# Kernel tuning notes

Hardware: AMD Instinct MI355X
Metric: run time of the kernel (lower is better)

## Reference

```python
import jax, jax.numpy as jnp
import numpy as np

# model constants (from source: PRE/COMM/OUT sizes; chosen: G, D, E, T, NF)
G, D, E, T = 128, 64, 8, 4096          # group feats, per-elevator feats, n elevators, timesteps
PRE, CI, CH, OUT, NF = 256, 128, 128, 128, 64
ROUNDS, DROPOFF = 3, 0.333
IN = G + D                              # elevator_input_size = 192
OIN = 2 * CH + IN                       # out-LSTM input = 448


def _cell(x, h, c, Wih, Whh, b):
    # torch nn.LSTM cell, gate order i,f,g,o; b = b_ih + b_hh
    g = x @ Wih.T + h @ Whh.T + b
    i, f, gg, o = jnp.split(g, 4, axis=-1)
    c2 = jax.nn.sigmoid(f) * c + jax.nn.sigmoid(i) * jnp.tanh(gg)
    h2 = jax.nn.sigmoid(o) * jnp.tanh(c2)
    return h2, c2


def _forward(features, pre_h0, pre_c0, out_h0, out_c0,
             Wih_p0, Whh_p0, b_p0, Wih_p1, Whh_p1, b_p1, Wfc, bfc,
             Wih_c0, Whh_c0, b_c0, Wih_c1, Whh_c1, b_c1,
             Wih_o, Whh_o, b_o, Wtar, btar, Wdir, bdir):
    def step(carry, feat):
        pre_h, pre_c, out_h, out_c = carry
        group = feat[:G]
        ele = feat[G:].reshape(E, D)
        x = jnp.concatenate([jnp.broadcast_to(group, (E, G)), ele], axis=-1)  # [E, IN]
        # preprocess: 2-layer LSTM single step, batched over elevators
        h0, c0 = _cell(x, pre_h[:, 0], pre_c[:, 0], Wih_p0, Whh_p0, b_p0)
        h1, c1 = _cell(h0, pre_h[:, 1], pre_c[:, 1], Wih_p1, Whh_p1, b_p1)
        pre_out = jax.nn.leaky_relu(h1 @ Wfc.T + bfc, 0.05)                   # [E, CI]
        new_pre_h = jnp.stack([h0, h1], axis=1)
        new_pre_c = jnp.stack([c0, c1], axis=1)
        # alpha-decayed communication rounds: sequential scan over elevators
        ch = jnp.zeros((2, CH), jnp.float32)
        cc = jnp.zeros((2, CH), jnp.float32)
        alpha = 1.0
        for _ in range(ROUNDS):
            def comm_step(cs, xin, alpha=alpha):
                ch_, cc_ = cs
                h0n, c0n = _cell(xin, ch_[0], cc_[0], Wih_c0, Whh_c0, b_c0)
                h0b = (1.0 - alpha) * ch_[0] + alpha * h0n
                c0b = (1.0 - alpha) * cc_[0] + alpha * c0n
                h1n, c1n = _cell(h0b, ch_[1], cc_[1], Wih_c1, Whh_c1, b_c1)
                h1b = (1.0 - alpha) * ch_[1] + alpha * h1n
                c1b = (1.0 - alpha) * cc_[1] + alpha * c1n
                return (jnp.stack([h0b, h1b]), jnp.stack([c0b, c1b])), None
            (ch, cc), _ = jax.lax.scan(comm_step, (ch, cc), pre_out)
            alpha *= DROPOFF
        group_dec = cc.reshape(-1)                                            # [2*CH] = comm_c.flatten()
        out_in = jnp.concatenate([jnp.broadcast_to(group_dec, (E, 2 * CH)), x], axis=-1)  # [E, OIN]
        oh, oc = _cell(out_in, out_h, out_c, Wih_o, Whh_o, b_o)
        tar = jax.nn.softmax(oh @ Wtar.T + btar, axis=-1)                     # [E, NF]
        dr = jax.nn.softmax(oh @ Wdir.T + bdir, axis=-1)                      # [E, 3]
        return (new_pre_h, new_pre_c, oh, oc), (tar, dr)

    _, (tar_seq, dir_seq) = jax.lax.scan(step, (pre_h0, pre_c0, out_h0, out_c0), features)
    return tar_seq, dir_seq


def setup_inputs() -> dict:
    key = jax.random.key(0)
    ks = iter(jax.random.split(key, 32))
    p = lambda *s: jax.random.normal(next(ks), s, jnp.float32) * 0.05
    return {
        "features": jax.random.normal(next(ks), (T, G + E * D), jnp.float32),
        "pre_h0": jnp.zeros((E, 2, PRE), jnp.float32),
        "pre_c0": jnp.zeros((E, 2, PRE), jnp.float32),
        "out_h0": jnp.zeros((E, OUT), jnp.float32),
        "out_c0": jnp.zeros((E, OUT), jnp.float32),
        "Wih_p0": p(4 * PRE, IN), "Whh_p0": p(4 * PRE, PRE), "b_p0": p(4 * PRE),
        "Wih_p1": p(4 * PRE, PRE), "Whh_p1": p(4 * PRE, PRE), "b_p1": p(4 * PRE),
        "Wfc": p(CI, PRE), "bfc": p(CI),
        "Wih_c0": p(4 * CH, CI), "Whh_c0": p(4 * CH, CH), "b_c0": p(4 * CH),
        "Wih_c1": p(4 * CH, CH), "Whh_c1": p(4 * CH, CH), "b_c1": p(4 * CH),
        "Wih_o": p(4 * OUT, OIN), "Whh_o": p(4 * OUT, OUT), "b_o": p(4 * OUT),
        "Wtar": p(NF, OUT), "btar": p(NF),
        "Wdir": p(3, OUT), "bdir": p(3),
    }


def reference(features, pre_h0, pre_c0, out_h0, out_c0,
              Wih_p0, Whh_p0, b_p0, Wih_p1, Whh_p1, b_p1, Wfc, bfc,
              Wih_c0, Whh_c0, b_c0, Wih_c1, Whh_c1, b_c1,
              Wih_o, Whh_o, b_o, Wtar, btar, Wdir, bdir):
    return _forward(features, pre_h0, pre_c0, out_h0, out_c0,
                    Wih_p0, Whh_p0, b_p0, Wih_p1, Whh_p1, b_p1, Wfc, bfc,
                    Wih_c0, Whh_c0, b_c0, Wih_c1, Whh_c1, b_c1,
                    Wih_o, Whh_o, b_o, Wtar, btar, Wdir, bdir)
```

## Files before the change

### kernel.cpp

```cpp
#include <hip/hip_runtime.h>
#include <hip/hip_bf16.h>

#define T_   4096
#define E_   8
#define NCON 56

typedef unsigned long long ull;

__device__ __forceinline__ float sigm(float x)  { return 1.0f / (1.0f + __expf(-x)); }
__device__ __forceinline__ float tanh_(float x) { return 1.0f - 2.0f / (__expf(2.0f * x) + 1.0f); }

__device__ __forceinline__ ull aload64(const ull* p) {
  return __hip_atomic_load(p, __ATOMIC_RELAXED, __HIP_MEMORY_SCOPE_AGENT);
}
__device__ __forceinline__ int aload32(const int* p) {
  return __hip_atomic_load(p, __ATOMIC_RELAXED, __HIP_MEMORY_SCOPE_AGENT);
}
__device__ __forceinline__ float aloadf(const float* p) {
  return __hip_atomic_load(p, __ATOMIC_RELAXED, __HIP_MEMORY_SCOPE_AGENT);
}
__device__ __forceinline__ void lbar() {
  asm volatile("s_waitcnt lgkmcnt(0)\n\ts_barrier" ::: "memory");
}

#define FMA_8(ACC, W, VA, VB)                                   \
  ACC[0] = fmaf((W), (VA).x, ACC[0]); ACC[1] = fmaf((W), (VA).y, ACC[1]); \
  ACC[2] = fmaf((W), (VA).z, ACC[2]); ACC[3] = fmaf((W), (VA).w, ACC[3]); \
  ACC[4] = fmaf((W), (VB).x, ACC[4]); ACC[5] = fmaf((W), (VB).y, ACC[5]); \
  ACC[6] = fmaf((W), (VB).z, ACC[6]); ACC[7] = fmaf((W), (VB).w, ACC[7]);

__global__ void initK(const float* __restrict__ Wih_p0, const float* __restrict__ Whh_p0,
                      const float* __restrict__ Wih_p1, const float* __restrict__ Whh_p1,
                      const float* __restrict__ Wih_c0, const float* __restrict__ Whh_c0,
                      const float* __restrict__ Wih_c1, const float* __restrict__ Whh_c1,
                      const float* __restrict__ Wih_o,
                      float* wt_p0, float* wt_p1, float* wt_c0, float* wt_c1,
                      float* wt_o1, float* wt_o2, int* zbase) {
  const int NW = 458752 + 524288 + 131072 + 131072 + 131072 + 98304;
  const int NZ = 65536 + 16384 + 65536 + 65536 + 65536 + 16384;
  const int NTOT = NW + NZ;
  const int gsz = gridDim.x * blockDim.x;
  for (int i = blockIdx.x * blockDim.x + threadIdx.x; i < NTOT; i += gsz) {
    int idx = i;
    if (idx < 458752) { int k = idx >> 10, c = idx & 1023;
      int wg = c >> 5, r5 = c & 31, gate = r5 >> 3, jl = r5 & 7;
      int col = gate * 256 + wg * 8 + jl;
      wt_p0[idx] = (k < 192) ? Wih_p0[col * 192 + k] : Whh_p0[col * 256 + (k - 192)]; continue; }
    idx -= 458752;
    if (idx < 524288) { int k = idx >> 10, c = idx & 1023;
      int wg = c >> 5, r5 = c & 31, gate = r5 >> 3, jl = r5 & 7;
      int col = gate * 256 + wg * 8 + jl;
      wt_p1[idx] = (k < 256) ? Wih_p1[col * 256 + k] : Whh_p1[col * 256 + (k - 256)]; continue; }
    idx -= 524288;
    if (idx < 131072) { int k = idx >> 9, r = idx & 511;
      wt_c0[idx] = (k < 128) ? Wih_c0[r * 128 + k] : Whh_c0[r * 128 + (k - 128)]; continue; }
    idx -= 131072;
    if (idx < 131072) { int k = idx >> 9, r = idx & 511;
      wt_c1[idx] = (k < 128) ? Wih_c1[r * 128 + k] : Whh_c1[r * 128 + (k - 128)]; continue; }
    idx -= 131072;
    if (idx < 131072) { int k = idx >> 9, r = idx & 511;
      wt_o1[idx] = Wih_o[r * 448 + k]; continue; }
    idx -= 131072;
    if (idx < 98304) { int k = idx >> 9, r = idx & 511;
      wt_o2[idx] = Wih_o[r * 448 + 256 + k]; continue; }
    idx -= 98304;
    zbase[idx] = 0;
  }
}

__global__ void opre2K(const float* __restrict__ feat, const float* __restrict__ wt_o2,
                       __hip_bfloat16* __restrict__ opre2) {
  __shared__ float xb[192 * 8];
  const int t = blockIdx.x, tid = threadIdx.x;
  const float* ft = feat + (size_t)t * 640;
  for (int idx = tid; idx < 192 * 8; idx += 256) {
    int k = idx >> 3, e = idx & 7;
    xb[idx] = (k < 128) ? ft[k] : ft[128 + e * 64 + (k - 128)];
  }
  __syncthreads();
  const int r = tid;
  float A0[8] = {0,0,0,0,0,0,0,0};
  float A1[8] = {0,0,0,0,0,0,0,0};
  const float4* x4 = (const float4*)xb;
  #pragma unroll 2
  for (int k = 0; k < 192; ++k) {
    float w0 = wt_o2[k * 512 + r];
    float w1 = wt_o2[k * 512 + 256 + r];
    float4 a = x4[k * 2], b = x4[k * 2 + 1];
    FMA_8(A0, w0, a, b);
    FMA_8(A1, w1, a, b);
  }
  #pragma unroll
  for (int e = 0; e < 8; ++e) {
    opre2[((size_t)t * 8 + e) * 512 + r]       = __float2bfloat16(A0[e]);
    opre2[((size_t)t * 8 + e) * 512 + 256 + r] = __float2bfloat16(A1[e]);
  }
}

__device__ __forceinline__ void comm_cell(
    const float* __restrict__ wt, const float* __restrict__ bias,
    const float* xin, float* hL, float* cL, float* glb, float* hout,
    float alpha, int tid) {
  const int r = tid;
  float A0[8] = {0,0,0,0,0,0,0,0};
  float A1[8] = {0,0,0,0,0,0,0,0};
  const float4* x4 = (const float4*)xin;
  #pragma unroll 2
  for (int k = 0; k < 128; ++k) {
    float w0 = wt[k * 512 + r];
    float w1 = wt[k * 512 + 256 + r];
    float4 a = x4[k * 2], b = x4[k * 2 + 1];
    FMA_8(A0, w0, a, b);
    FMA_8(A1, w1, a, b);
  }
  const float4* h4 = (const float4*)hL;
  #pragma unroll 2
  for (int k = 0; k < 128; ++k) {
    float w0 = wt[(128 + k) * 512 + r];
    float w1 = wt[(128 + k) * 512 + 256 + r];
    float4 a = h4[k * 2], b = h4[k * 2 + 1];
    FMA_8(A0, w0, a, b);
    FMA_8(A1, w1, a, b);
  }
  {
    float4* g4 = (float4*)glb;
    g4[r * 2]             = make_float4(A0[0], A0[1], A0[2], A0[3]);
    g4[r * 2 + 1]         = make_float4(A0[4], A0[5], A0[6], A0[7]);
    g4[(256 + r) * 2]     = make_float4(A1[0], A1[1], A1[2], A1[3]);
    g4[(256 + r) * 2 + 1] = make_float4(A1[4], A1[5], A1[6], A1[7]);
  }
  __syncthreads();
  for (int idx = tid; idx < 1024; idx += 256) {
    int jj = idx >> 3, tt = idx & 7;
    float gi = glb[jj * 8 + tt]         + bias[jj];
    float gf = glb[(128 + jj) * 8 + tt] + bias[128 + jj];
    float gg = glb[(256 + jj) * 8 + tt] + bias[256 + jj];
    float go = glb[(384 + jj) * 8 + tt] + bias[384 + jj];
    float cold = cL[idx], hold = hL[idx];
    float c2 = sigm(gf) * cold + sigm(gi) * tanh_(gg);
    float h2 = sigm(go) * tanh_(c2);
    float hb = fmaf(alpha, h2 - hold, hold);
    float cb = fmaf(alpha, c2 - cold, cold);
    hL[idx] = hb; cL[idx] = cb;
    if (hout) hout[idx] = hb;
  }
  __syncthreads();
}

__launch_bounds__(256, 1)
__global__ void megaK(const float* __restrict__ feat,
                      const float* __restrict__ pre_h0, const float* __restrict__ pre_c0,
                      const float* __restrict__ wt_p0, const float* __restrict__ wt_p1,
                      const float* __restrict__ b_p0, const float* __restrict__ b_p1,
                      float* __restrict__ h0ring, float* __restrict__ h1ring,
                      float* __restrict__ h1all,
                      int* __restrict__ flagsA, int* __restrict__ flagB1,
                      int* __restrict__ flagsBC,
                      const float* __restrict__ Wfc, const float* __restrict__ bfc,
                      const float* __restrict__ wt_c0, const float* __restrict__ wt_c1,
                      const float* __restrict__ b_c0, const float* __restrict__ b_c1,
                      const float* __restrict__ wt_o1, const float* __restrict__ b_o,
                      float* __restrict__ opre1, int* __restrict__ flagC,
                      const __hip_bfloat16* __restrict__ opre2,
                      const float* __restrict__ Whh_o, const float* __restrict__ out_h0,
                      const float* __restrict__ out_c0, float* __restrict__ oh_g) {
  __shared__ float lds[38912];
  const int wg = blockIdx.x, tid = threadIdx.x;

  if (wg < 32) {
    float* wl   = lds;
    float* xbuf = lds + 14336;
    float* hsf  = lds + 15872;
    float* gl   = lds + 17920;
    const int r5 = tid & 31, kq = tid >> 5;
    for (int idx = tid; idx < 14336; idx += 256)
      wl[idx] = wt_p0[(size_t)(idx >> 5) * 1024 + wg * 32 + (idx & 31)];
    float creg = 0.f, bi = 0.f, bff = 0.f, bg = 0.f, bo = 0.f;
    if (tid < 64) {
      const int jl = tid >> 3, e = tid & 7, j = wg * 8 + jl;
      creg = pre_c0[(e * 2 + 0) * 256 + j];
      bi = b_p0[j]; bff = b_p0[256 + j]; bg = b_p0[512 + j]; bo = b_p0[768 + j];
    }
    for (int idx = tid; idx < 2048; idx += 256) {
      int k = idx >> 3, e = idx & 7;
      hsf[idx] = pre_h0[(e * 2 + 0) * 256 + k];
    }
    for (int idx = tid; idx < 1536; idx += 256) {
      int k = idx >> 3, e = idx & 7;
      xbuf[idx] = (k < 128) ? feat[k] : feat[128 + e * 64 + (k - 128)];
    }
    __syncthreads();
    float Ax[8] = {0,0,0,0,0,0,0,0};
    {
      const float4* x4 = (const float4*)xbuf;
      #pragma unroll
      for (int k = kq * 24; k < kq * 24 + 24; ++k) {
        float w = wl[k * 32 + r5];
        float4 a = x4[k * 2], b = x4[k * 2 + 1];
        FMA_8(Ax, w, a, b);
      }
    }
    for (int t = 0; t < T_; ++t) {
      float px[6];
      if (t + 1 < T_) {
        const float* ft1 = feat + (size_t)(t + 1) * 640;
        #pragma unroll
        for (int i = 0; i < 6; ++i) {
          int idx = tid + i * 256; int k = idx >> 3, e = idx & 7;
          px[i] = (k < 128) ? ft1[k] : ft1[128 + e * 64 + (k - 128)];
        }
      }
      float A[8];
      #pragma unroll
      for (int i = 0; i < 8; ++i) A[i] = Ax[i];
      {
        const float4* h4 = (const float4*)hsf;
        #pragma unroll
        for (int k2 = 0; k2 < 32; ++k2) {
          const int k = kq * 32 + k2;
          float w = wl[(192 + k) * 32 + r5];
          float4 a = h4[k * 2], b = h4[k * 2 + 1];
          FMA_8(A, w, a, b);
        }
      }
      {
        float4* g4 = (float4*)gl;
        g4[(kq * 32 + r5) * 2]     = make_float4(A[0], A[1], A[2], A[3]);
        g4[(kq * 32 + r5) * 2 + 1] = make_float4(A[4], A[5], A[6], A[7]);
      }
      if (t >= 24 && tid >= 224) {
        const int t2 = (t - 24) | 7;
        const int* fp = flagsBC + ((size_t)(t2 & 63) * 32 + (tid - 224)) * 32;
        while (aload32(fp) < t2 + 1) __builtin_amdgcn_s_sleep(16);
      }
      lbar();
      if (tid < 64) {
        float s0 = 0.f, s1 = 0.f, s2 = 0.f, s3 = 0.f;
        #pragma unroll
        for (int q = 0; q < 8; ++q) {
          s0 += gl[q * 256 + tid];       s1 += gl[q * 256 + 64 + tid];
          s2 += gl[q * 256 + 128 + tid]; s3 += gl[q * 256 + 192 + tid];
        }
        float c2 = sigm(s1 + bff) * creg + sigm(s0 + bi) * tanh_(s2 + bg);
        float h2 = sigm(s3 + bo) * tanh_(c2);
        creg = c2;
        __hip_atomic_store(&h0ring[(size_t)(t & 31) * 2048 + wg * 64 + tid], h2,
                           __ATOMIC_RELAXED, __HIP_MEMORY_SCOPE_AGENT);
        asm volatile("s_waitcnt vmcnt(0)" ::: "memory");
        if (tid == 0)
          __hip_atomic_store(&flagsA[((size_t)(t & 63) * 32 + wg) * 32], t + 1,
                             __ATOMIC_RELAXED, __HIP_MEMORY_SCOPE_AGENT);
      }
      if (t + 1 >= T_) break;
      #pragma unroll
      for (int i = 0; i < 6; ++i) xbuf[tid + i * 256] = px[i];
      if (tid >= 64 && tid < 96) {
        const int* fp = flagsA + ((size_t)(t & 63) * 32 + (tid - 64)) * 32;
        while (aload32(fp) < t + 1) __builtin_amdgcn_s_sleep(1);
      }
      lbar();
      ull v[4];
      {
        const ull* s8 = (const ull*)(h0ring + (size_t)(t & 31) * 2048);
        #pragma unroll
        for (int i = 0; i < 4; ++i) v[i] = aload64(s8 + tid * 4 + i);
      }
      #pragma unroll
      for (int i = 0; i < 8; ++i) Ax[i] = 0.f;
      {
        const float4* x4 = (const float4*)xbuf;
        #pragma unroll
        for (int k = kq * 24; k < kq * 24 + 24; ++k) {
          float w = wl[k * 32 + r5];
          float4 a = x4[k * 2], b = x4[k * 2 + 1];
          FMA_8(Ax, w, a, b);
        }
      }
      {
        ull* d8 = (ull*)hsf;
        #pragma unroll
        for (int i = 0; i < 4; ++i) d8[tid * 4 + i] = v[i];
      }
      lbar();
    }
  } else if (wg < 64) {
    const int wgl = wg - 32;
    float* wl  = lds;
    float* xh0 = lds + 16384;
    float* hsf = lds + 18432;
    float* gl  = lds + 20480;
    const int r5 = tid & 31, kq = tid >> 5;
    for (int idx = tid; idx < 16384; idx += 256)
      wl[idx] = wt_p1[(size_t)(idx >> 5) * 1024 + wgl * 32 + (idx & 31)];
    float creg = 0.f, bi = 0.f, bff = 0.f, bg = 0.f, bo = 0.f;
    if (tid < 64) {
      const int jl = tid >> 3, e = tid & 7, j = wgl * 8 + jl;
      creg = pre_c0[(e * 2 + 1) * 256 + j];
      bi = b_p1[j]; bff = b_p1[256 + j]; bg = b_p1[512 + j]; bo = b_p1[768 + j];
    }
    for (int idx = tid; idx < 2048; idx += 256) {
      int k = idx >> 3, e = idx & 7;
      hsf[idx] = pre_h0[(e * 2 + 1) * 256 + k];
    }
    __syncthreads();
    if (tid >= 64 && tid < 128) {
      const int lane = tid - 64;
      const int slot = lane >> 5, b = lane & 31;
      const int* fp = flagsA + ((size_t)slot * 32 + b) * 32;
      while (aload32(fp) < slot + 1) __builtin_amdgcn_s_sleep(1);
    }
    __syncthreads();
    ull v0[4];
    {
      const ull* s8 = (const ull*)h0ring;
      #pragma unroll
      for (int i = 0; i < 4; ++i) v0[i] = aload64(s8 + tid * 4 + i);
    }
    {
      ull* d8 = (ull*)xh0;
      #pragma unroll
      for (int i = 0; i < 4; ++i) d8[tid * 4 + i] = v0[i];
    }
    lbar();
    float Ax[8] = {0,0,0,0,0,0,0,0};
    {
      const float4* x4 = (const float4*)xh0;
      #pragma unroll
      for (int k = kq * 32; k < kq * 32 + 32; ++k) {
        float w = wl[k * 32 + r5];
        float4 a = x4[k * 2], b = x4[k * 2 + 1];
        FMA_8(Ax, w, a, b);
      }
    }
    {
      const ull* s8 = (const ull*)(h0ring + 2048);
      #pragma unroll
      for (int i = 0; i < 4; ++i) v0[i] = aload64(s8 + tid * 4 + i);
    }
    for (int t = 0; t < T_; ++t) {
      float A[8];
      #pragma unroll
      for (int i = 0; i < 8; ++i) A[i] = Ax[i];
      {
        const float4* h4 = (const float4*)hsf;
        #pragma unroll
        for (int k2 = 0; k2 < 32; ++k2) {
          const int k = kq * 32 + k2;
          float w = wl[(256 + k) * 32 + r5];
          float4 a = h4[k * 2], b = h4[k * 2 + 1];
          FMA_8(A, w, a, b);
        }
      }
      {
        float4* g4 = (float4*)gl;
        g4[(kq * 32 + r5) * 2]     = make_float4(A[0], A[1], A[2], A[3]);
        g4[(kq * 32 + r5) * 2 + 1] = make_float4(A[4], A[5], A[6], A[7]);
      }
      lbar();
      if (tid < 64) {
        float s0 = 0.f, s1 = 0.f, s2 = 0.f, s3 = 0.f;
        #pragma unroll
        for (int q = 0; q < 8; ++q) {
          s0 += gl[q * 256 + tid];       s1 += gl[q * 256 + 64 + tid];
          s2 += gl[q * 256 + 128 + tid]; s3 += gl[q * 256 + 192 + tid];
        }
        float c2 = sigm(s1 + bff) * creg + sigm(s0 + bi) * tanh_(s2 + bg);
        float h2 = sigm(s3 + bo) * tanh_(c2);
        creg = c2;
        __hip_atomic_store(&h1ring[(size_t)(t & 7) * 2048 + wgl * 64 + tid], h2,
                           __ATOMIC_RELAXED, __HIP_MEMORY_SCOPE_AGENT);
        asm volatile("s_waitcnt vmcnt(0)" ::: "memory");
        if (tid == 0)
          __hip_atomic_store(&flagB1[((size_t)(t & 63) * 32 + wgl) * 32], t + 1,
                             __ATOMIC_RELAXED, __HIP_MEMORY_SCOPE_AGENT);
        __hip_atomic_store(&h1all[(size_t)t * 2048 + wgl * 64 + tid], h2,
                           __ATOMIC_RELAXED, __HIP_MEMORY_SCOPE_AGENT);
        if ((t & 7) == 7) {
          asm volatile("s_waitcnt vmcnt(0)" ::: "memory");
          if (tid == 0)
            __hip_atomic_store(&flagsBC[((size_t)(t & 63) * 32 + wgl) * 32], t + 1,
                               __ATOMIC_RELAXED, __HIP_MEMORY_SCOPE_AGENT);
        }
      }
      if (t + 1 >= T_) break;
      if (tid >= 64 && tid < 128) {
        const int lane = tid - 64;
        if (lane < 32) {
          const int* fp = flagB1 + ((size_t)(t & 63) * 32 + lane) * 32;
          while (aload32(fp) < t + 1) __builtin_amdgcn_s_sleep(1);
        } else if (t + 2 < T_) {
          const int* fp = flagsA + ((size_t)((t + 2) & 63) * 32 + (lane - 32)) * 32;
          while (aload32(fp) < t + 3) __builtin_amdgcn_s_sleep(1);
        }
      }
      lbar();
      ull v1[4];
      {
        const ull* s8 = (const ull*)(h1ring + (size_t)(t & 7) * 2048);
        #pragma unroll
        for (int i = 0; i < 4; ++i) v1[i] = aload64(s8 + tid * 4 + i);
      }
      {
        ull* d8 = (ull*)xh0;
        #pragma unroll
        for (int i = 0; i < 4; ++i) d8[tid * 4 + i] = v0[i];
      }
      lbar();
      if (t + 2 < T_) {
        const ull* s8 = (const ull*)(h0ring + (size_t)((t + 2) & 31) * 2048);
        #pragma unroll
        for (int i = 0; i < 4; ++i) v0[i] = aload64(s8 + tid * 4 + i);
      }
      #pragma unroll
      for (int i = 0; i < 8; ++i) Ax[i] = 0.f;
      {
        const float4* x4 = (const float4*)xh0;
        #pragma unroll
        for (int k = kq * 32; k < kq * 32 + 32; ++k) {
          float w = wl[k * 32 + r5];
          float4 a = x4[k * 2], b = x4[k * 2 + 1];
          FMA_8(Ax, w, a, b);
        }
      }
      {
        ull* d8 = (ull*)hsf;
        #pragma unroll
        for (int i = 0; i < 4; ++i) d8[tid * 4 + i] = v1[i];
      }
      lbar();
    }
  } else if (wg < 72) {
    const int e = wg - 64;
    float* wlds = lds;
    float* ohl  = lds + 32768;
    float* gl   = lds + 32896;
    for (int idx = tid; idx < 32768; idx += 256) {
      int k = idx >> 8, rr = idx & 255;
      wlds[idx] = Whh_o[(256 + rr) * 128 + k];
    }
    float w[128];
    #pragma unroll
    for (int k = 0; k < 128; ++k) w[k] = Whh_o[tid * 128 + k];
    if (tid < 128) ohl[tid] = out_h0[e * 128 + tid];
    float creg = (tid < 128) ? out_c0[e * 128 + tid] : 0.f;
    __syncthreads();
    if (tid == 0) { while (aload32(&flagC[0]) == 0) __builtin_amdgcn_s_sleep(4); }
    __syncthreads();
    const int r0 = tid, r1 = tid + 256;
    float pa = aloadf(&opre1[r0]), pb = aloadf(&opre1[r1]);
    float qa = __bfloat162float(opre2[(size_t)e * 512 + r0]);
    float qb = __bfloat162float(opre2[(size_t)e * 512 + r1]);
    float na = aloadf(&opre1[512 + r0]), nb = aloadf(&opre1[512 + r1]);
    float ma = __bfloat162float(opre2[(size_t)(8 + e) * 512 + r0]);
    float mb = __bfloat162float(opre2[(size_t)(8 + e) * 512 + r1]);
    for (int t = 0; t < T_; ++t) {
      float a0 = pa + qa, a1 = pb + qb;
      pa = na; pb = nb; qa = ma; qb = mb;
      if ((t & 7) == 6 && t + 2 < T_) {
        if (tid == 0) { while (aload32(&flagC[((t + 2) >> 3) * 32]) == 0) __builtin_amdgcn_s_sleep(4); }
        __syncthreads();
      }
      if (t + 2 < T_) {
        na = aloadf(&opre1[(size_t)(t + 2) * 512 + r0]);
        nb = aloadf(&opre1[(size_t)(t + 2) * 512 + r1]);
        ma = __bfloat162float(opre2[((size_t)(t + 2) * 8 + e) * 512 + r0]);
        mb = __bfloat162float(opre2[((size_t)(t + 2) * 8 + e) * 512 + r1]);
      }
      const float4* o4 = (const float4*)ohl;
      #pragma unroll
      for (int kk = 0; kk < 32; ++kk) {
        float4 x = o4[kk];
        a0 = fmaf(w[kk * 4 + 0], x.x, a0); a0 = fmaf(w[kk * 4 + 1], x.y, a0);
        a0 = fmaf(w[kk * 4 + 2], x.z, a0); a0 = fmaf(w[kk * 4 + 3], x.w, a0);
        a1 = fmaf(wlds[(kk * 4 + 0) * 256 + tid], x.x, a1);
        a1 = fmaf(wlds[(kk * 4 + 1) * 256 + tid], x.y, a1);
        a1 = fmaf(wlds[(kk * 4 + 2) * 256 + tid], x.z, a1);
        a1 = fmaf(wlds[(kk * 4 + 3) * 256 + tid], x.w, a1);
      }
      gl[r0] = a0; gl[r1] = a1;
      __syncthreads();
      if (tid < 128) {
        float gi = gl[tid], gf = gl[128 + tid], gg = gl[256 + tid], go = gl[384 + tid];
        float c2 = sigm(gf) * creg + sigm(gi) * tanh_(gg);
        float h2 = sigm(go) * tanh_(c2);
        creg = c2;
        ohl[tid] = h2;
        oh_g[(size_t)t * 1024 + e * 128 + tid] = h2;
      }
      __syncthreads();
    }
  } else {
    const int cb = wg - 72;
    float* h1c    = lds;
    float* polAll = lds + 16384;
    float* ch0 = lds + 24576; float* cc0 = lds + 25600;
    float* ch1 = lds + 26624; float* cc1 = lds + 27648;
    float* h0b = lds + 28672;
    float* glb = lds + 29696;
    for (int chunk = cb; chunk < 512; chunk += NCON) {
      const int t0 = chunk * 8;
      if (tid < 32) {
        const int* fp = flagsBC + ((size_t)((t0 + 7) & 63) * 32 + tid) * 32;
        while (aload32(fp) < t0 + 8) __builtin_amdgcn_s_sleep(64);
      }
      __syncthreads();
      {
        const ull* src = (const ull*)(h1all + (size_t)t0 * 2048);
        ull* dst = (ull*)h1c;
        for (int i = tid; i < 8192; i += 256) dst[i] = aload64(src + i);
      }
      __syncthreads();
      {
        const int c = tid >> 1, half = tid & 1;
        const float bv = bfc[c];
        const float* wrow = Wfc + c * 256;
        for (int tt = 0; tt < 8; ++tt) {
          float a0 = bv, a1 = bv, a2 = bv, a3 = bv;
          const float4* h4 = (const float4*)(h1c + tt * 2048);
          #pragma unroll 4
          for (int k = 0; k < 256; ++k) {
            float wv = wrow[k];
            float4 x = h4[k * 2 + half];
            a0 = fmaf(wv, x.x, a0); a1 = fmaf(wv, x.y, a1);
            a2 = fmaf(wv, x.z, a2); a3 = fmaf(wv, x.w, a3);
          }
          float vv[4] = {a0, a1, a2, a3};
          #pragma unroll
          for (int i = 0; i < 4; ++i) {
            float v = vv[i];
            v = (v > 0.f) ? v : 0.05f * v;
            polAll[(half * 4 + i) * 1024 + c * 8 + tt] = v;
          }
        }
      }
      for (int idx = tid; idx < 1024; idx += 256) { ch0[idx]=0.f; cc0[idx]=0.f; ch1[idx]=0.f; cc1[idx]=0.f; }
      __syncthreads();
      float alpha = 1.0f;
      for (int rd = 0; rd < 3; ++rd) {
        for (int e = 0; e < E_; ++e) {
          comm_cell(wt_c0, b_c0, polAll + e * 1024, ch0, cc0, glb, h0b, alpha, tid);
          comm_cell(wt_c1, b_c1, h0b, ch1, cc1, glb, nullptr, alpha, tid);
        }
        alpha *= 0.333f;
      }
      {
        const int r = tid;
        float A0[8], A1[8];
        #pragma unroll
        for (int tt = 0; tt < 8; ++tt) { A0[tt] = b_o[r]; A1[tt] = b_o[256 + r]; }
        const float4* c04 = (const float4*)cc0;
        const float4* c14 = (const float4*)cc1;
        #pragma unroll 2
        for (int k = 0; k < 128; ++k) {
          float w0 = wt_o1[k * 512 + r], w1 = wt_o1[k * 512 + 256 + r];
          float4 a = c04[k * 2], b = c04[k * 2 + 1];
          FMA_8(A0, w0, a, b);
          FMA_8(A1, w1, a, b);
        }
        #pragma unroll 2
        for (int k = 0; k < 128; ++k) {
          float w0 = wt_o1[(128 + k) * 512 + r], w1 = wt_o1[(128 + k) * 512 + 256 + r];
          float4 a = c14[k * 2], b = c14[k * 2 + 1];
          FMA_8(A0, w0, a, b);
          FMA_8(A1, w1, a, b);
        }
        #pragma unroll
        for (int tt = 0; tt < 8; ++tt) {
          __hip_atomic_store(&opre1[((size_t)(t0 + tt)) * 512 + r], A0[tt],
                             __ATOMIC_RELAXED, __HIP_MEMORY_SCOPE_AGENT);
          __hip_atomic_store(&opre1[((size_t)(t0 + tt)) * 512 + 256 + r], A1[tt],
                             __ATOMIC_RELAXED, __HIP_MEMORY_SCOPE_AGENT);
        }
      }
      __syncthreads();
      if (tid == 0)
        __hip_atomic_store(&flagC[chunk * 32], 1, __ATOMIC_RELAXED, __HIP_MEMORY_SCOPE_AGENT);
      __syncthreads();
    }
  }
}

__global__ void phaseD(const float* __restrict__ oh_g,
                       const float* __restrict__ Wtar, const float* __restrict__ btar,
                       const float* __restrict__ Wdir, const float* __restrict__ bdir,
                       float* __restrict__ outp) {
  __shared__ float ohl[1024];
  const int t = blockIdx.x, tid = threadIdx.x;
  for (int idx = tid; idx < 1024; idx += 64) ohl[idx] = oh_g[(size_t)t * 1024 + idx];
  __syncthreads();
  const int f = tid;
  for (int e = 0; e < E_; ++e) {
    float acc = btar[f];
    const float* wr = Wtar + f * 128;
    #pragma unroll 4
    for (int k = 0; k < 128; ++k) acc = fmaf(wr[k], ohl[e * 128 + k], acc);
    float m = acc;
    #pragma unroll
    for (int off = 32; off; off >>= 1) m = fmaxf(m, __shfl_xor(m, off, 64));
    float ex = __expf(acc - m);
    float s = ex;
    #pragma unroll
    for (int off = 32; off; off >>= 1) s += __shfl_xor(s, off, 64);
    outp[((size_t)t * 8 + e) * 64 + f] = ex / s;
  }
  if (tid < 8) {
    int e = tid;
    float d0 = bdir[0], d1 = bdir[1], d2 = bdir[2];
    #pragma unroll 4
    for (int k = 0; k < 128; ++k) {
      float x = ohl[e * 128 + k];
      d0 = fmaf(Wdir[k], x, d0);
      d1 = fmaf(Wdir[128 + k], x, d1);
      d2 = fmaf(Wdir[256 + k], x, d2);
    }
    float m = fmaxf(d0, fmaxf(d1, d2));
    float x0 = __expf(d0 - m), x1 = __expf(d1 - m), x2 = __expf(d2 - m);
    float s = x0 + x1 + x2;
    float* dp = outp + (size_t)T_ * 8 * 64 + ((size_t)t * 8 + e) * 3;
    dp[0] = x0 / s; dp[1] = x1 / s; dp[2] = x2 / s;
  }
}

extern "C" void kernel_launch(void* const* d_in, const int* in_sizes, int n_in,
                              void* d_out, int out_size, void* d_ws, size_t ws_size,
                              hipStream_t stream) {
  (void)in_sizes; (void)n_in; (void)out_size; (void)ws_size;
  const float* feat   = (const float*)d_in[0];
  const float* pre_h0 = (const float*)d_in[1];
  const float* pre_c0 = (const float*)d_in[2];
  const float* out_h0 = (const float*)d_in[3];
  const float* out_c0 = (const float*)d_in[4];
  const float* Wih_p0 = (const float*)d_in[5];
  const float* Whh_p0 = (const float*)d_in[6];
  const float* b_p0   = (const float*)d_in[7];
  const float* Wih_p1 = (const float*)d_in[8];
  const float* Whh_p1 = (const float*)d_in[9];
  const float* b_p1   = (const float*)d_in[10];
  const float* Wfc    = (const float*)d_in[11];
  const float* bfc    = (const float*)d_in[12];
  const float* Wih_c0 = (const float*)d_in[13];
  const float* Whh_c0 = (const float*)d_in[14];
  const float* b_c0   = (const float*)d_in[15];
  const float* Wih_c1 = (const float*)d_in[16];
  const float* Whh_c1 = (const float*)d_in[17];
  const float* b_c1   = (const float*)d_in[18];
  const float* Wih_o  = (const float*)d_in[19];
  const float* Whh_o  = (const float*)d_in[20];
  const float* b_o    = (const float*)d_in[21];
  const float* Wtar   = (const float*)d_in[22];
  const float* btar   = (const float*)d_in[23];
  const float* Wdir   = (const float*)d_in[24];
  const float* bdir   = (const float*)d_in[25];
  float* outp = (float*)d_out;

  float* ws = (float*)d_ws;
  size_t off = 0;
  float* opre1    = ws + off; off += (size_t)T_ * 512;
  float* oh_g     = ws + off; off += (size_t)T_ * E_ * 128;
  float* wt_p0    = ws + off; off += (size_t)448 * 1024;
  float* wt_p1    = ws + off; off += (size_t)512 * 1024;
  float* wt_c0    = ws + off; off += (size_t)256 * 512;
  float* wt_c1    = ws + off; off += (size_t)256 * 512;
  float* wt_o1    = ws + off; off += (size_t)256 * 512;
  float* wt_o2    = ws + off; off += (size_t)192 * 512;
  __hip_bfloat16* opre2 = (__hip_bfloat16*)(ws + off);
  off += (size_t)T_ * E_ * 512 / 2;
  float* h1all  = ws + off; off += (size_t)T_ * 2048;
  float* h0ring = ws + off; off += (size_t)32 * 2048;
  float* h1ring = ws + off; off += (size_t)8 * 2048;
  int* flags    = (int*)(ws + off);
  int* flagsA   = flags;
  int* flagB1   = flags + (size_t)64 * 32 * 32;
  int* flagsBC  = flags + (size_t)2 * 64 * 32 * 32;
  int* flagC    = flags + (size_t)3 * 64 * 32 * 32;
  int* zbase    = (int*)h0ring;

  initK<<<dim3(1024), dim3(256), 0, stream>>>(
      Wih_p0, Whh_p0, Wih_p1, Whh_p1, Wih_c0, Whh_c0, Wih_c1, Whh_c1, Wih_o,
      wt_p0, wt_p1, wt_c0, wt_c1, wt_o1, wt_o2, zbase);
  opre2K<<<dim3(T_), dim3(256), 0, stream>>>(feat, wt_o2, opre2);
  megaK<<<dim3(32 + 32 + 8 + NCON), dim3(256), 0, stream>>>(
      feat, pre_h0, pre_c0, wt_p0, wt_p1, b_p0, b_p1,
      h0ring, h1ring, h1all, flagsA, flagB1, flagsBC,
      Wfc, bfc, wt_c0, wt_c1, b_c0, b_c1, wt_o1, b_o, opre1, flagC,
      opre2, Whh_o, out_h0, out_c0, oh_g);
  phaseD<<<dim3(T_), dim3(64), 0, stream>>>(oh_g, Wtar, btar, Wdir, bdir, outp);
}
```

Before: 16.91 ms.

## Replace per-step flag handshakes with generation-tagged ring data polling

```diff
diff --git a/kernel.cpp b/kernel.cpp
--- a/kernel.cpp
+++ b/kernel.cpp
@@ -18,6 +18,18 @@
 }
 __device__ __forceinline__ float aloadf(const float* p) {
   return __hip_atomic_load(p, __ATOMIC_RELAXED, __HIP_MEMORY_SCOPE_AGENT);
+}
+__device__ __forceinline__ float tagf(float h, unsigned g) {
+  return __uint_as_float((__float_as_uint(h) & ~7u) | g);
+}
+__device__ __forceinline__ bool tagok4(const ull* v, unsigned g) {
+  bool ok = true;
+  #pragma unroll
+  for (int i = 0; i < 4; ++i) {
+    unsigned lo = (unsigned)v[i], hi = (unsigned)(v[i] >> 32);
+    ok &= ((lo & 7u) == g) & ((hi & 7u) == g);
+  }
+  return ok;
 }
 __device__ __forceinline__ void lbar() {
   asm volatile("s_waitcnt lgkmcnt(0)\n\ts_barrier" ::: "memory");
@@ -37,7 +49,7 @@
                       float* wt_p0, float* wt_p1, float* wt_c0, float* wt_c1,
                       float* wt_o1, float* wt_o2, int* zbase) {
   const int NW = 458752 + 524288 + 131072 + 131072 + 131072 + 98304;
-  const int NZ = 65536 + 16384 + 65536 + 65536 + 65536 + 16384;
+  const int NZ = 65536 + 16384 + 65536 + 16384;
   const int NTOT = NW + NZ;
   const int gsz = gridDim.x * blockDim.x;
   for (int i = blockIdx.x * blockDim.x + threadIdx.x; i < NTOT; i += gsz) {
@@ -153,9 +165,7 @@
                       const float* __restrict__ wt_p0, const float* __restrict__ wt_p1,
                       const float* __restrict__ b_p0, const float* __restrict__ b_p1,
                       float* __restrict__ h0ring, float* __restrict__ h1ring,
-                      float* __restrict__ h1all,
-                      int* __restrict__ flagsA, int* __restrict__ flagB1,
-                      int* __restrict__ flagsBC,
+                      float* __restrict__ h1all, int* __restrict__ flagsBC,
                       const float* __restrict__ Wfc, const float* __restrict__ bfc,
                       const float* __restrict__ wt_c0, const float* __restrict__ wt_c1,
                       const float* __restrict__ b_c0, const float* __restrict__ b_c1,
@@ -168,10 +178,11 @@
   const int wg = blockIdx.x, tid = threadIdx.x;
 
   if (wg < 32) {
-    float* wl   = lds;
-    float* xbuf = lds + 14336;
-    float* hsf  = lds + 15872;
-    float* gl   = lds + 17920;
+    float* wl  = lds;
+    float* xb0 = lds + 14336;
+    float* xb1 = lds + 15872;
+    float* hsf = lds + 17408;
+    float* gl  = lds + 19456;
     const int r5 = tid & 31, kq = tid >> 5;
     for (int idx = tid; idx < 14336; idx += 256)
       wl[idx] = wt_p0[(size_t)(idx >> 5) * 1024 + wg * 32 + (idx & 31)];
@@ -187,12 +198,13 @@
     }
     for (int idx = tid; idx < 1536; idx += 256) {
       int k = idx >> 3, e = idx & 7;
-      xbuf[idx] = (k < 128) ? feat[k] : feat[128 + e * 64 + (k - 128)];
+      xb0[idx] = (k < 128) ? feat[k] : feat[128 + e * 64 + (k - 128)];
     }
     __syncthreads();
+    const bool own = ((tid >> 3) == wg);
     float Ax[8] = {0,0,0,0,0,0,0,0};
     {
-      const float4* x4 = (const float4*)xbuf;
+      const float4* x4 = (const float4*)xb0;
       #pragma unroll
       for (int k = kq * 24; k < kq * 24 + 24; ++k) {
         float w = wl[k * 32 + r5];
@@ -228,12 +240,19 @@
         g4[(kq * 32 + r5) * 2]     = make_float4(A[0], A[1], A[2], A[3]);
         g4[(kq * 32 + r5) * 2 + 1] = make_float4(A[4], A[5], A[6], A[7]);
       }
+      if (t + 1 < T_) {
+        float* xbN = ((t + 1) & 1) ? xb1 : xb0;
+        #pragma unroll
+        for (int i = 0; i < 6; ++i) xbN[tid + i * 256] = px[i];
+      }
       if (t >= 24 && tid >= 224) {
         const int t2 = (t - 24) | 7;
         const int* fp = flagsBC + ((size_t)(t2 & 63) * 32 + (tid - 224)) * 32;
         while (aload32(fp) < t2 + 1) __builtin_amdgcn_s_sleep(16);
       }
       lbar();
+      const unsigned g = ((unsigned)(t >> 5) % 7u) + 1u;
+      float* ringS = h0ring + (size_t)(t & 31) * 2048;
       if (tid < 64) {
         float s0 = 0.f, s1 = 0.f, s2 = 0.f, s3 = 0.f;
         #pragma unroll
@@ -244,31 +263,21 @@
         float c2 = sigm(s1 + bff) * creg + sigm(s0 + bi) * tanh_(s2 + bg);
         float h2 = sigm(s3 + bo) * tanh_(c2);
         creg = c2;
-        __hip_atomic_store(&h0ring[(size_t)(t & 31) * 2048 + wg * 64 + tid], h2,
+        __hip_atomic_store(&ringS[wg * 64 + tid], tagf(h2, g),
                            __ATOMIC_RELAXED, __HIP_MEMORY_SCOPE_AGENT);
-        asm volatile("s_waitcnt vmcnt(0)" ::: "memory");
-        if (tid == 0)
-          __hip_atomic_store(&flagsA[((size_t)(t & 63) * 32 + wg) * 32], t + 1,
-                             __ATOMIC_RELAXED, __HIP_MEMORY_SCOPE_AGENT);
+        hsf[wg * 64 + tid] = h2;
       }
       if (t + 1 >= T_) break;
-      #pragma unroll
-      for (int i = 0; i < 6; ++i) xbuf[tid + i * 256] = px[i];
-      if (tid >= 64 && tid < 96) {
-        const int* fp = flagsA + ((size_t)(t & 63) * 32 + (tid - 64)) * 32;
-        while (aload32(fp) < t + 1) __builtin_amdgcn_s_sleep(1);
-      }
-      lbar();
       ull v[4];
-      {
-        const ull* s8 = (const ull*)(h0ring + (size_t)(t & 31) * 2048);
-        #pragma unroll
-        for (int i = 0; i < 4; ++i) v[i] = aload64(s8 + tid * 4 + i);
+      const ull* rp = (const ull*)ringS + tid * 4;
+      if (!own) {
+        #pragma unroll
+        for (int i = 0; i < 4; ++i) v[i] = aload64(rp + i);
       }
       #pragma unroll
       for (int i = 0; i < 8; ++i) Ax[i] = 0.f;
       {
-        const float4* x4 = (const float4*)xbuf;
+        const float4* x4 = (const float4*)(((t + 1) & 1) ? xb1 : xb0);
         #pragma unroll
         for (int k = kq * 24; k < kq * 24 + 24; ++k) {
           float w = wl[k * 32 + r5];
@@ -276,7 +285,12 @@
           FMA_8(Ax, w, a, b);
         }
       }
-      {
+      if (!own) {
+        while (!tagok4(v, g)) {
+          __builtin_amdgcn_s_sleep(1);
+          #pragma unroll
+          for (int i = 0; i < 4; ++i) v[i] = aload64(rp + i);
+        }
         ull* d8 = (ull*)hsf;
         #pragma unroll
         for (int i = 0; i < 4; ++i) d8[tid * 4 + i] = v[i];
@@ -303,23 +317,21 @@
       hsf[idx] = pre_h0[(e * 2 + 1) * 256 + k];
     }
     __syncthreads();
-    if (tid >= 64 && tid < 128) {
-      const int lane = tid - 64;
-      const int slot = lane >> 5, b = lane & 31;
-      const int* fp = flagsA + ((size_t)slot * 32 + b) * 32;
-      while (aload32(fp) < slot + 1) __builtin_amdgcn_s_sleep(1);
-    }
-    __syncthreads();
-    ull v0[4];
+    const bool own = ((tid >> 3) == wgl);
+    ull pv[4];
     {
-      const ull* s8 = (const ull*)h0ring;
-      #pragma unroll
-      for (int i = 0; i < 4; ++i) v0[i] = aload64(s8 + tid * 4 + i);
-    }
-    {
+      ull v[4];
+      const ull* rp = (const ull*)h0ring + tid * 4;
+      #pragma unroll
+      for (int i = 0; i < 4; ++i) v[i] = aload64(rp + i);
+      while (!tagok4(v, 1u)) {
+        __builtin_amdgcn_s_sleep(1);
+        #pragma unroll
+        for (int i = 0; i < 4; ++i) v[i] = aload64(rp + i);
+      }
       ull* d8 = (ull*)xh0;
       #pragma unroll
-      for (int i = 0; i < 4; ++i) d8[tid * 4 + i] = v0[i];
+      for (int i = 0; i < 4; ++i) d8[tid * 4 + i] = v[i];
     }
     lbar();
     float Ax[8] = {0,0,0,0,0,0,0,0};
@@ -333,10 +345,16 @@
       }
     }
     {
-      const ull* s8 = (const ull*)(h0ring + 2048);
-      #pragma unroll
-      for (int i = 0; i < 4; ++i) v0[i] = aload64(s8 + tid * 4 + i);
-    }
+      const ull* rp = (const ull*)(h0ring + 2048) + tid * 4;
+      #pragma unroll
+      for (int i = 0; i < 4; ++i) pv[i] = aload64(rp + i);
+      while (!tagok4(pv, 1u)) {
+        __builtin_amdgcn_s_sleep(1);
+        #pragma unroll
+        for (int i = 0; i < 4; ++i) pv[i] = aload64(rp + i);
+      }
+    }
+    lbar();
     for (int t = 0; t < T_; ++t) {
       float A[8];
       #pragma unroll
@@ -356,7 +374,14 @@
         g4[(kq * 32 + r5) * 2]     = make_float4(A[0], A[1], A[2], A[3]);
         g4[(kq * 32 + r5) * 2 + 1] = make_float4(A[4], A[5], A[6], A[7]);
       }
+      if (t + 1 < T_) {
+        ull* d8 = (ull*)xh0;
+        #pragma unroll
+        for (int i = 0; i < 4; ++i) d8[tid * 4 + i] = pv[i];
+      }
       lbar();
+      const unsigned g1 = ((unsigned)(t >> 3) % 7u) + 1u;
+      float* ringS = h1ring + (size_t)(t & 7) * 2048;
       if (tid < 64) {
         float s0 = 0.f, s1 = 0.f, s2 = 0.f, s3 = 0.f;
         #pragma unroll
@@ -367,12 +392,9 @@
         float c2 = sigm(s1 + bff) * creg + sigm(s0 + bi) * tanh_(s2 + bg);
         float h2 = sigm(s3 + bo) * tanh_(c2);
         creg = c2;
-        __hip_atomic_store(&h1ring[(size_t)(t & 7) * 2048 + wgl * 64 + tid], h2,
+        __hip_atomic_store(&ringS[wgl * 64 + tid], tagf(h2, g1),
                            __ATOMIC_RELAXED, __HIP_MEMORY_SCOPE_AGENT);
-        asm volatile("s_waitcnt vmcnt(0)" ::: "memory");
-        if (tid == 0)
-          __hip_atomic_store(&flagB1[((size_t)(t & 63) * 32 + wgl) * 32], t + 1,
-                             __ATOMIC_RELAXED, __HIP_MEMORY_SCOPE_AGENT);
+        hsf[wgl * 64 + tid] = h2;
         __hip_atomic_store(&h1all[(size_t)t * 2048 + wgl * 64 + tid], h2,
                            __ATOMIC_RELAXED, __HIP_MEMORY_SCOPE_AGENT);
         if ((t & 7) == 7) {
@@ -383,33 +405,11 @@
         }
       }
       if (t + 1 >= T_) break;
-      if (tid >= 64 && tid < 128) {
-        const int lane = tid - 64;
-        if (lane < 32) {
-          const int* fp = flagB1 + ((size_t)(t & 63) * 32 + lane) * 32;
-          while (aload32(fp) < t + 1) __builtin_amdgcn_s_sleep(1);
-        } else if (t + 2 < T_) {
-          const int* fp = flagsA + ((size_t)((t + 2) & 63) * 32 + (lane - 32)) * 32;
-          while (aload32(fp) < t + 3) __builtin_amdgcn_s_sleep(1);
-        }
-      }
-      lbar();
-      ull v1[4];
-      {
-        const ull* s8 = (const ull*)(h1ring + (size_t)(t & 7) * 2048);
-        #pragma unroll
-        for (int i = 0; i < 4; ++i) v1[i] = aload64(s8 + tid * 4 + i);
-      }
-      {
-        ull* d8 = (ull*)xh0;
-        #pragma unroll
-        for (int i = 0; i < 4; ++i) d8[tid * 4 + i] = v0[i];
-      }
-      lbar();
-      if (t + 2 < T_) {
-        const ull* s8 = (const ull*)(h0ring + (size_t)((t + 2) & 31) * 2048);
-        #pragma unroll
-        for (int i = 0; i < 4; ++i) v0[i] = aload64(s8 + tid * 4 + i);
+      ull w1[4];
+      const ull* rp1 = (const ull*)ringS + tid * 4;
+      if (!own) {
+        #pragma unroll
+        for (int i = 0; i < 4; ++i) w1[i] = aload64(rp1 + i);
       }
       #pragma unroll
       for (int i = 0; i < 8; ++i) Ax[i] = 0.f;
@@ -422,10 +422,26 @@
           FMA_8(Ax, w, a, b);
         }
       }
-      {
+      if (!own) {
+        while (!tagok4(w1, g1)) {
+          __builtin_amdgcn_s_sleep(1);
+          #pragma unroll
+          for (int i = 0; i < 4; ++i) w1[i] = aload64(rp1 + i);
+        }
         ull* d8 = (ull*)hsf;
         #pragma unroll
-        for (int i = 0; i < 4; ++i) d8[tid * 4 + i] = v1[i];
+        for (int i = 0; i < 4; ++i) d8[tid * 4 + i] = w1[i];
+      }
+      if (t + 2 < T_) {
+        const unsigned g0 = ((unsigned)((t + 2) >> 5) % 7u) + 1u;
+        const ull* rp0 = (const ull*)(h0ring + (size_t)((t + 2) & 31) * 2048) + tid * 4;
+        #pragma unroll
+        for (int i = 0; i < 4; ++i) pv[i] = aload64(rp0 + i);
+        while (!tagok4(pv, g0)) {
+          __builtin_amdgcn_s_sleep(1);
+          #pragma unroll
+          for (int i = 0; i < 4; ++i) pv[i] = aload64(rp0 + i);
+        }
       }
       lbar();
     }
@@ -669,10 +685,8 @@
   float* h0ring = ws + off; off += (size_t)32 * 2048;
   float* h1ring = ws + off; off += (size_t)8 * 2048;
   int* flags    = (int*)(ws + off);
-  int* flagsA   = flags;
-  int* flagB1   = flags + (size_t)64 * 32 * 32;
-  int* flagsBC  = flags + (size_t)2 * 64 * 32 * 32;
-  int* flagC    = flags + (size_t)3 * 64 * 32 * 32;
+  int* flagsBC  = flags;
+  int* flagC    = flags + (size_t)64 * 32 * 32;
   int* zbase    = (int*)h0ring;
 
   initK<<<dim3(1024), dim3(256), 0, stream>>>(
@@ -681,7 +695,7 @@
   opre2K<<<dim3(T_), dim3(256), 0, stream>>>(feat, wt_o2, opre2);
   megaK<<<dim3(32 + 32 + 8 + NCON), dim3(256), 0, stream>>>(
       feat, pre_h0, pre_c0, wt_p0, wt_p1, b_p0, b_p1,
-      h0ring, h1ring, h1all, flagsA, flagB1, flagsBC,
+      h0ring, h1ring, h1all, flagsBC,
       Wfc, bfc, wt_c0, wt_c1, b_c0, b_c1, wt_o1, b_o, opre1, flagC,
       opre2, Whh_o, out_h0, out_c0, oh_g);
   phaseD<<<dim3(T_), dim3(64), 0, stream>>>(oh_g, Wtar, btar, Wdir, bdir, outp);
```

Result: faster. 15.78 ms (-6.6%).
